# Performance work log

Hardware: AMD Instinct MI355X
Metric: run time of the kernel (lower is better)

## Reference

```python
import jax, jax.numpy as jnp
import numpy as np

NUM_HEADS = 8
NUM_GROUPS = 8
EPS = 1e-5


def group_norm(x, gamma, beta):
    # x: [B, C, H, W], 8 groups over channel dim
    B, C, H, W = x.shape
    xg = x.reshape(B, NUM_GROUPS, C // NUM_GROUPS, H, W)
    mean = xg.mean(axis=(2, 3, 4), keepdims=True)
    var = xg.var(axis=(2, 3, 4), keepdims=True)
    xn = ((xg - mean) * jax.lax.rsqrt(var + EPS)).reshape(B, C, H, W)
    return xn * gamma[None, :, None, None] + beta[None, :, None, None]


def conv1x1(x, w, b):
    # w: [O, C] (1x1 conv kernel squeezed), x: [B, C, H, W]
    return jnp.einsum('oc,bchw->bohw', w, x) + b[None, :, None, None]


def setup_inputs() -> dict:
    key = jax.random.key(0)
    ks = jax.random.split(key, 6)
    B, C, H, W = 16, 512, 32, 32
    x = jax.random.normal(ks[0], (B, C, H, W), dtype=jnp.float32)
    norm_w = jnp.ones((C,), jnp.float32)
    norm_b = jnp.zeros((C,), jnp.float32)
    s = 1.0 / np.sqrt(C)
    qkv_w = jax.random.uniform(ks[1], (3 * C, C), jnp.float32, -s, s)
    qkv_b = jax.random.uniform(ks[2], (3 * C,), jnp.float32, -s, s)
    proj_w = jax.random.uniform(ks[3], (C, C), jnp.float32, -s, s)
    proj_b = jax.random.uniform(ks[4], (C,), jnp.float32, -s, s)
    return {"x": x, "norm_w": norm_w, "norm_b": norm_b,
            "qkv_w": qkv_w, "qkv_b": qkv_b, "proj_w": proj_w, "proj_b": proj_b}


def reference(x, norm_w, norm_b, qkv_w, qkv_b, proj_w, proj_b):
    B, C, H, W = x.shape
    hd = C // NUM_HEADS  # head dim
    h = group_norm(x, norm_w, norm_b)
    qkv = conv1x1(h, qkv_w, qkv_b)                 # [B, 3C, H, W]
    q, k, v = jnp.split(qkv, 3, axis=1)
    q = q.reshape(B, NUM_HEADS, hd, H * W)
    k = k.reshape(B, NUM_HEADS, hd, H * W)
    v = v.reshape(B, NUM_HEADS, hd, H * W)
    scale = hd ** (-0.5)
    attn = jax.nn.softmax(jnp.einsum('bhci,bhcj->bhij', q, k) * scale, axis=-1)
    h = jnp.einsum('bhij,bhcj->bhci', attn, v).reshape(B, C, H, W)
    h = conv1x1(h, proj_w, proj_b)
    return x + h
```

## Files before the change

### kernel.cpp

```cpp
#include <hip/hip_runtime.h>
#include <hip/hip_bf16.h>


typedef __bf16 bf16;
typedef __attribute__((ext_vector_type(8))) __bf16 bf16x8;
typedef __attribute__((ext_vector_type(4))) float f32x4;
typedef __attribute__((ext_vector_type(16))) float f32x16;
typedef __attribute__((ext_vector_type(4))) unsigned int u32x4;

#define SCALE_Q 0.18033688f

__device__ __forceinline__ bf16x8 ld8(const bf16* p) {
    return *reinterpret_cast<const bf16x8*>(p);
}

__device__ __forceinline__ void gl_lds16(const void* g, void* l) {
    __builtin_amdgcn_global_load_lds(
        (const __attribute__((address_space(1))) void*)g,
        (__attribute__((address_space(3))) void*)l, 16, 0, 0);
}

__global__ __launch_bounds__(256) void cvt_weights(const float* __restrict__ qkv_w,
                                                   const float* __restrict__ proj_w,
                                                   bf16* __restrict__ dst) {
    const int N1 = 1536 * 512;
    int i = (blockIdx.x * 256 + threadIdx.x) * 4;
    float4 f = (i < N1) ? *reinterpret_cast<const float4*>(qkv_w + i)
                        : *reinterpret_cast<const float4*>(proj_w + (i - N1));
    dst[i + 0] = (bf16)f.x;
    dst[i + 1] = (bf16)f.y;
    dst[i + 2] = (bf16)f.z;
    dst[i + 3] = (bf16)f.w;
}

__global__ __launch_bounds__(256) void gn_fused(const float* __restrict__ x,
                                                const float* __restrict__ gamma,
                                                const float* __restrict__ beta,
                                                bf16* __restrict__ hnT) {
    int bg = blockIdx.x;
    int b = bg >> 3, g = bg & 7;
    const float* base = x + (size_t)bg * 65536;
    int t = threadIdx.x;
    int wave = t >> 6, lane = t & 63;

    float s = 0.f, sq = 0.f;
    for (int i = t * 4; i < 65536; i += 256 * 4) {
        float4 f = *reinterpret_cast<const float4*>(base + i);
        s += f.x + f.y + f.z + f.w;
        sq += f.x * f.x + f.y * f.y + f.z * f.z + f.w * f.w;
    }
    #pragma unroll
    for (int off = 32; off > 0; off >>= 1) {
        s += __shfl_down(s, off);
        sq += __shfl_down(sq, off);
    }
    __shared__ float ls[4], lq[4];
    __shared__ float2 st;
    if (lane == 0) { ls[wave] = s; lq[wave] = sq; }
    __syncthreads();
    if (t == 0) {
        s = ls[0] + ls[1] + ls[2] + ls[3];
        sq = lq[0] + lq[1] + lq[2] + lq[3];
        float mean = s * (1.f / 65536.f);
        float var = sq * (1.f / 65536.f) - mean * mean;
        st = make_float2(mean, rsqrtf(var + 1e-5f));
    }
    __syncthreads();
    float mean = st.x, rstd = st.y;

    __shared__ float tile[64][65];
    int cl = t & 63;
    float ga = gamma[g * 64 + cl] * rstd;
    float be = beta[g * 64 + cl] - mean * ga;
    for (int pt = 0; pt < 16; pt++) {
        const float* xb = base + pt * 64;
        #pragma unroll
        for (int r = 0; r < 16; r++) {
            int crow = r * 4 + (t >> 6);
            tile[crow][t & 63] = xb[(size_t)crow * 1024 + (t & 63)];
        }
        __syncthreads();
        bf16* ob = hnT + ((size_t)b * 1024 + pt * 64) * 512 + g * 64 + cl;
        #pragma unroll
        for (int r = 0; r < 16; r++) {
            int pl = r * 4 + (t >> 6);
            ob[(size_t)pl * 512] = (bf16)(tile[cl][pl] * ga + be);
        }
        __syncthreads();
    }
}

__device__ __forceinline__ void gemm_stage(const bf16* __restrict__ A,
                                           const bf16* __restrict__ B,
                                           char* smem, int buf,
                                           int m_blk, int n_blk, int k0,
                                           int wave, int lane) {
    char* Al = smem + buf * 32768;
    char* Bl = Al + 16384;
    #pragma unroll
    for (int i = 0; i < 4; i++) {
        int seg = i * 4 + wave;
        int r = seg * 8 + (lane >> 3);
        int cg = (lane & 7) ^ (r & 7);
        gl_lds16((const char*)(A + (size_t)(m_blk + r) * 512 + k0) + cg * 16,
                 Al + seg * 1024);
        gl_lds16((const char*)(B + (size_t)(n_blk + r) * 512 + k0) + cg * 16,
                 Bl + seg * 1024);
    }
}

__device__ __forceinline__ void gemm_compute(const char* smem, int buf,
                                             int wave, int lane,
                                             f32x4 (&acc)[4][4]) {
    const char* Al = smem + buf * 32768;
    const char* Bl = Al + 16384;
    int l15 = lane & 15, hi = lane >> 4;
    int mb = (wave >> 1) * 64, nb = (wave & 1) * 64;
    #pragma unroll
    for (int kc = 0; kc < 2; kc++) {
        int ck = kc * 4 + hi;
        bf16x8 a[4], b[4];
        #pragma unroll
        for (int mf = 0; mf < 4; mf++) {
            int row = mb + mf * 16 + l15;
            a[mf] = *reinterpret_cast<const bf16x8*>(Al + row * 128 + (ck ^ (row & 7)) * 16);
        }
        #pragma unroll
        for (int nf = 0; nf < 4; nf++) {
            int row = nb + nf * 16 + l15;
            b[nf] = *reinterpret_cast<const bf16x8*>(Bl + row * 128 + (ck ^ (row & 7)) * 16);
        }
        #pragma unroll
        for (int mf = 0; mf < 4; mf++)
            #pragma unroll
            for (int nf = 0; nf < 4; nf++)
                acc[mf][nf] = __builtin_amdgcn_mfma_f32_16x16x32_bf16(
                    a[mf], b[nf], acc[mf][nf], 0, 0, 0);
    }
}

#define GEMM_LDS_LOOP(A_, B_, SMEM_)                            \
    f32x4 acc[4][4] = {};                                       \
    {                                                           \
        gemm_stage(A_, B_, SMEM_, 0, m_blk, n_blk, 0, wave, lane); \
        __syncthreads();                                        \
        int buf = 0;                                            \
        for (int ks = 0; ks < 8; ks++) {                        \
            if (ks < 7)                                         \
                gemm_stage(A_, B_, SMEM_, buf ^ 1, m_blk, n_blk, (ks + 1) * 64, wave, lane); \
            gemm_compute(SMEM_, buf, wave, lane, acc);          \
            __syncthreads();                                    \
            buf ^= 1;                                           \
        }                                                       \
    }

__global__ __launch_bounds__(256, 2) void gemm_qkv(const bf16* __restrict__ hnT,
                                                   const bf16* __restrict__ wqkv,
                                                   const float* __restrict__ qkv_b,
                                                   bf16* __restrict__ qk_t,
                                                   bf16* __restrict__ vbuf) {
    __shared__ char smem[65536];
    int b = blockIdx.z;
    int wave = threadIdx.x >> 6, lane = threadIdx.x & 63;
    int l15 = lane & 15;
    int y = blockIdx.y;
    if (y < 8) {
        int m_blk = blockIdx.x * 128;
        int n_blk = y * 128;
        const bf16* A = hnT + (size_t)b * 1024 * 512;
        GEMM_LDS_LOOP(A, wqkv, smem)
        bf16* out = qk_t + (size_t)b * 1024 * 1024;
        int col0 = n_blk + (wave & 1) * 64 + l15;
        int row0 = m_blk + (wave >> 1) * 64 + (lane >> 4) * 4;
        #pragma unroll
        for (int nf = 0; nf < 4; nf++) {
            int col = col0 + nf * 16;
            float bias = qkv_b[col];
            float scl = (col < 512) ? SCALE_Q : 1.0f;
            #pragma unroll
            for (int mf = 0; mf < 4; mf++)
                #pragma unroll
                for (int r = 0; r < 4; r++)
                    out[(size_t)(row0 + mf * 16 + r) * 1024 + col] =
                        (bf16)((acc[mf][nf][r] + bias) * scl);
        }
    } else {
        int m_blk = (y - 8) * 128;
        int n_blk = blockIdx.x * 128;
        const bf16* A = wqkv + (size_t)1024 * 512;
        const bf16* Bm = hnT + (size_t)b * 1024 * 512;
        GEMM_LDS_LOOP(A, Bm, smem)
        bf16* out = vbuf + (size_t)b * 512 * 1024;
        int col0 = n_blk + (wave & 1) * 64 + l15;
        int row0 = m_blk + (wave >> 1) * 64 + (lane >> 4) * 4;
        #pragma unroll
        for (int mf = 0; mf < 4; mf++)
            #pragma unroll
            for (int r = 0; r < 4; r++) {
                int row = row0 + mf * 16 + r;
                float bias = qkv_b[1024 + row];
                #pragma unroll
                for (int nf = 0; nf < 4; nf++)
                    out[(size_t)row * 1024 + col0 + nf * 16] = (bf16)(acc[mf][nf][r] + bias);
            }
    }
}

__global__ __launch_bounds__(256, 2) void gemm_proj(const bf16* __restrict__ wproj,
                                                    const bf16* __restrict__ attnT,
                                                    const float* __restrict__ proj_b,
                                                    const float* __restrict__ x,
                                                    float* __restrict__ out) {
    __shared__ char smem[65536];
    int b = blockIdx.z;
    int wave = threadIdx.x >> 6, lane = threadIdx.x & 63;
    int m_blk = blockIdx.x * 128;
    int n_blk = blockIdx.y * 128;
    const bf16* Bm = attnT + (size_t)b * 1024 * 512;
    GEMM_LDS_LOOP(wproj, Bm, smem)
    const float* xb = x + (size_t)b * 512 * 1024;
    float* ob = out + (size_t)b * 512 * 1024;
    int l15 = lane & 15;
    int col0 = n_blk + (wave & 1) * 64 + l15;
    int row0 = m_blk + (wave >> 1) * 64 + (lane >> 4) * 4;
    #pragma unroll
    for (int mf = 0; mf < 4; mf++)
        #pragma unroll
        for (int r = 0; r < 4; r++) {
            int row = row0 + mf * 16 + r;
            float bias = proj_b[row];
            #pragma unroll
            for (int nf = 0; nf < 4; nf++) {
                size_t idx = (size_t)row * 1024 + col0 + nf * 16;
                ob[idx] = acc[mf][nf][r] + bias + xb[idx];
            }
        }
}

__global__ __launch_bounds__(256, 2) void attn_kernel(const bf16* __restrict__ qk_t,
                                                      const bf16* __restrict__ vbuf,
                                                      bf16* __restrict__ attnT) {
    int flat = blockIdx.x;
    int it = flat >> 7;
    int bh = flat & 127;
    int b = bh >> 3, h = bh & 7;
    int wave = threadIdx.x >> 6, lane = threadIdx.x & 63;
    int l31 = lane & 31, hi = lane >> 5;
    int i0 = it * 128 + wave * 32;
    const bf16* qkb = qk_t + (size_t)b * 1024 * 1024;
    const bf16* kbase = qkb + 512 + h * 64;
    const bf16* vb = vbuf + ((size_t)b * 512 + h * 64) * 1024;

    __shared__ __align__(16) char smem[32768];

    bf16x8 bq[4];
    #pragma unroll
    for (int kc = 0; kc < 4; kc++)
        bq[kc] = ld8(qkb + (size_t)(i0 + l31) * 1024 + h * 64 + kc * 16 + hi * 8);

    f32x16 oacc[2] = {};
    f32x4 l4 = {};

    int srow = wave * 8 + (lane >> 3);
    int cg = (lane & 7) ^ (lane >> 3);
    const char* kp = (const char*)kbase + (size_t)srow * 2048 + cg * 16;
    const char* vp = (const char*)vb + (size_t)srow * 2048 + cg * 16;
    char* ldsK = smem + wave * 1024;

#define ATTN_STAGE(BUFI)                                     \
    {                                                        \
        gl_lds16(kp,         ldsK + (BUFI) * 16384);         \
        gl_lds16(kp + 65536, ldsK + (BUFI) * 16384 + 4096);  \
        gl_lds16(vp,         ldsK + (BUFI) * 16384 + 8192);  \
        gl_lds16(vp + 65536, ldsK + (BUFI) * 16384 + 12288); \
        kp += 131072;                                        \
        vp += 128;                                           \
    }

    int rx = l31 & 7;
    int vaddr[4];
    #pragma unroll
    for (int k = 0; k < 4; k++) vaddr[k] = l31 * 128 + (((k * 2 + hi) ^ rx) * 16);

#define ATTN_COMPUTE(BUFC)                                                              \
    {                                                                                   \
        bf16x8 kf[2][4];                                                                \
        _Pragma("unroll")                                                               \
        for (int jb = 0; jb < 2; jb++)                                                  \
            _Pragma("unroll")                                                           \
            for (int kc = 0; kc < 4; kc++)                                              \
                kf[jb][kc] = *reinterpret_cast<const bf16x8*>(                          \
                    smem + (BUFC) * 16384 + jb * 4096 + vaddr[kc]);                     \
        f32x16 s[2] = {};                                                               \
        _Pragma("unroll")                                                               \
        for (int kc = 0; kc < 4; kc++) {                                                \
            s[0] = __builtin_amdgcn_mfma_f32_32x32x16_bf16(kf[0][kc], bq[kc], s[0], 0, 0, 0); \
            s[1] = __builtin_amdgcn_mfma_f32_32x32x16_bf16(kf[1][kc], bq[kc], s[1], 0, 0, 0); \
        }                                                                               \
        bf16x8 vf[2][4];                                                                \
        _Pragma("unroll")                                                               \
        for (int df = 0; df < 2; df++)                                                  \
            _Pragma("unroll")                                                           \
            for (int ks = 0; ks < 4; ks++)                                              \
                vf[df][ks] = *reinterpret_cast<const bf16x8*>(                          \
                    smem + (BUFC) * 16384 + 8192 + df * 4096 + vaddr[ks]);              \
        unsigned int pk0[2][4], pk1[2][4];                                              \
        _Pragma("unroll")                                                               \
        for (int jb = 0; jb < 2; jb++)                                                  \
            _Pragma("unroll")                                                           \
            for (int m = 0; m < 4; m++) {                                               \
                float e0 = exp2f(s[jb][m * 4 + 0]);                                     \
                float e1 = exp2f(s[jb][m * 4 + 1]);                                     \
                float e2 = exp2f(s[jb][m * 4 + 2]);                                     \
                float e3 = exp2f(s[jb][m * 4 + 3]);                                     \
                f32x4 ev = {e0, e1, e2, e3};                                            \
                l4 += ev;                                                               \
                asm("v_cvt_pk_bf16_f32 %0, %1, %2" : "=v"(pk0[jb][m]) : "v"(e0), "v"(e1)); \
                asm("v_cvt_pk_bf16_f32 %0, %1, %2" : "=v"(pk1[jb][m]) : "v"(e2), "v"(e3)); \
            }                                                                           \
        bf16x8 af[4];                                                                   \
        _Pragma("unroll")                                                               \
        for (int jb = 0; jb < 2; jb++)                                                  \
            _Pragma("unroll")                                                           \
            for (int tt = 0; tt < 2; tt++) {                                            \
                unsigned int a0 = pk0[jb][tt * 2], b0 = pk0[jb][tt * 2 + 1];            \
                unsigned int a1 = pk1[jb][tt * 2], b1 = pk1[jb][tt * 2 + 1];            \
                asm("v_permlane32_swap_b32 %0, %1" : "+v"(a0), "+v"(b0));               \
                asm("v_permlane32_swap_b32 %0, %1" : "+v"(a1), "+v"(b1));               \
                u32x4 w = {a0, a1, b0, b1};                                             \
                af[jb * 2 + tt] = __builtin_bit_cast(bf16x8, w);                        \
            }                                                                           \
        _Pragma("unroll")                                                               \
        for (int ks = 0; ks < 4; ks++) {                                                \
            oacc[0] = __builtin_amdgcn_mfma_f32_32x32x16_bf16(af[ks], vf[0][ks], oacc[0], 0, 0, 0); \
            oacc[1] = __builtin_amdgcn_mfma_f32_32x32x16_bf16(af[ks], vf[1][ks], oacc[1], 0, 0, 0); \
        }                                                                               \
    }

    ATTN_STAGE(0)

    for (int t = 0; t < 16; t += 2) {
        asm volatile("" ::: "memory");
        __builtin_amdgcn_s_barrier();
        ATTN_STAGE(1)
        asm volatile("s_waitcnt vmcnt(4)" ::: "memory");
        __builtin_amdgcn_s_barrier();
        asm volatile("" ::: "memory");
        ATTN_COMPUTE(0)

        asm volatile("" ::: "memory");
        __builtin_amdgcn_s_barrier();
        if (t < 14) {
            ATTN_STAGE(0)
            asm volatile("s_waitcnt vmcnt(4)" ::: "memory");
        } else {
            asm volatile("s_waitcnt vmcnt(0)" ::: "memory");
        }
        __builtin_amdgcn_s_barrier();
        asm volatile("" ::: "memory");
        ATTN_COMPUTE(1)
    }
#undef ATTN_STAGE
#undef ATTN_COMPUTE

    float l_part = (l4[0] + l4[1]) + (l4[2] + l4[3]);
    float lsum = l_part + __shfl_xor(l_part, 32);
    float inv = 1.f / lsum;

    __syncthreads();

    bf16* O_l = (bf16*)smem;
    #pragma unroll
    for (int reg = 0; reg < 16; reg++) {
        int qrow = (reg & 3) + 8 * (reg >> 2) + 4 * hi;
        float iv = __shfl(inv, qrow);
        O_l[(wave * 32 + qrow) * 72 + l31]      = (bf16)(oacc[0][reg] * iv);
        O_l[(wave * 32 + qrow) * 72 + 32 + l31] = (bf16)(oacc[1][reg] * iv);
    }
    __syncthreads();
    {
        int tt = threadIdx.x;
        int il = tt >> 1, half = tt & 1;
        const bf16* lsrc = O_l + il * 72 + half * 32;
        bf16* gdst = attnT + ((size_t)b * 1024 + it * 128 + il) * 512 + h * 64 + half * 32;
        #pragma unroll
        for (int k = 0; k < 4; k++)
            *reinterpret_cast<bf16x8*>(gdst + k * 8) =
                *reinterpret_cast<const bf16x8*>(lsrc + k * 8);
    }
}

extern "C" void kernel_launch(void* const* d_in, const int* in_sizes, int n_in,
                              void* d_out, int out_size, void* d_ws, size_t ws_size,
                              hipStream_t stream) {
    (void)in_sizes; (void)n_in; (void)out_size; (void)ws_size;
    const float* x      = (const float*)d_in[0];
    const float* norm_w = (const float*)d_in[1];
    const float* norm_b = (const float*)d_in[2];
    const float* qkv_w  = (const float*)d_in[3];
    const float* qkv_b  = (const float*)d_in[4];
    const float* proj_w = (const float*)d_in[5];
    const float* proj_b = (const float*)d_in[6];
    float* out = (float*)d_out;

    char* w = (char*)d_ws;
    bf16* wqkv  = (bf16*)w;
    bf16* wproj = wqkv + (size_t)1536 * 512;
    bf16* hnT   = wproj + (size_t)512 * 512;
    bf16* qk_t  = hnT + (size_t)16 * 1024 * 512;
    bf16* vbuf  = qk_t + (size_t)16 * 1024 * 1024;
    bf16* attnT = vbuf + (size_t)16 * 512 * 1024;

    cvt_weights<<<1024, 256, 0, stream>>>(qkv_w, proj_w, wqkv);
    gn_fused<<<128, 256, 0, stream>>>(x, norm_w, norm_b, hnT);
    gemm_qkv<<<dim3(8, 12, 16), 256, 0, stream>>>(hnT, wqkv, qkv_b, qk_t, vbuf);
    attn_kernel<<<1024, 256, 0, stream>>>(qk_t, vbuf, attnT);
    gemm_proj<<<dim3(4, 8, 16), 256, 0, stream>>>(wproj, attnT, proj_b, x, out);
}
```

Measured before the change: 145.9 us.

## Fuse weight conversion into single-pass group norm with LDS-cached bf16 input

Merges the separate weight-conversion kernel into the group-norm kernel, with each of the 128 blocks converting an 8192-element slice of the weights. The group norm now reads x from global memory once instead of twice. Each block stages the whole group as bf16 in 128KB of dynamic LDS with an XOR swizzle, then does the transposed normalized write from LDS. This removes one launch and one read of x, but the large LDS allocation limits occupancy to one block per CU and adds bf16 rounding before normalization.

```diff
diff --git a/kernel.cpp b/kernel.cpp
--- a/kernel.cpp
+++ b/kernel.cpp
@@ -20,73 +20,81 @@
         (__attribute__((address_space(3))) void*)l, 16, 0, 0);
 }
 
-__global__ __launch_bounds__(256) void cvt_weights(const float* __restrict__ qkv_w,
-                                                   const float* __restrict__ proj_w,
-                                                   bf16* __restrict__ dst) {
-    const int N1 = 1536 * 512;
-    int i = (blockIdx.x * 256 + threadIdx.x) * 4;
-    float4 f = (i < N1) ? *reinterpret_cast<const float4*>(qkv_w + i)
-                        : *reinterpret_cast<const float4*>(proj_w + (i - N1));
-    dst[i + 0] = (bf16)f.x;
-    dst[i + 1] = (bf16)f.y;
-    dst[i + 2] = (bf16)f.z;
-    dst[i + 3] = (bf16)f.w;
-}
-
-__global__ __launch_bounds__(256) void gn_fused(const float* __restrict__ x,
-                                                const float* __restrict__ gamma,
-                                                const float* __restrict__ beta,
-                                                bf16* __restrict__ hnT) {
+__global__ __launch_bounds__(256) void gn_cvt_onepass(const float* __restrict__ x,
+                                                      const float* __restrict__ gamma,
+                                                      const float* __restrict__ beta,
+                                                      bf16* __restrict__ hnT,
+                                                      const float* __restrict__ qkv_w,
+                                                      const float* __restrict__ proj_w,
+                                                      bf16* __restrict__ wdst) {
+    extern __shared__ char dsm[];
+    bf16* xc = (bf16*)dsm;
+    float* red = (float*)(dsm + 131072);
     int bg = blockIdx.x;
     int b = bg >> 3, g = bg & 7;
     const float* base = x + (size_t)bg * 65536;
-    int t = threadIdx.x;
-    int wave = t >> 6, lane = t & 63;
+    int t = threadIdx.x, wave = t >> 6, lane = t & 63;
+
+    {
+        const float* src = (bg < 96) ? qkv_w + bg * 8192 : proj_w + (bg - 96) * 8192;
+        bf16* dst = wdst + (size_t)bg * 8192;
+        #pragma unroll
+        for (int k = 0; k < 8; k++) {
+            int i = k * 1024 + t * 4;
+            float4 f = *reinterpret_cast<const float4*>(src + i);
+            dst[i + 0] = (bf16)f.x;
+            dst[i + 1] = (bf16)f.y;
+            dst[i + 2] = (bf16)f.z;
+            dst[i + 3] = (bf16)f.w;
+        }
+    }
 
     float s = 0.f, sq = 0.f;
-    for (int i = t * 4; i < 65536; i += 256 * 4) {
-        float4 f = *reinterpret_cast<const float4*>(base + i);
-        s += f.x + f.y + f.z + f.w;
-        sq += f.x * f.x + f.y * f.y + f.z * f.z + f.w * f.w;
+    {
+        int pc = t >> 1, half = t & 1;
+        for (int k = 0; k < 64; k++) {
+            float4 f = *reinterpret_cast<const float4*>(base + (size_t)k * 1024 + t * 4);
+            s += (f.x + f.y) + (f.z + f.w);
+            sq += (f.x * f.x + f.y * f.y) + (f.z * f.z + f.w * f.w);
+            unsigned pk0, pk1;
+            asm("v_cvt_pk_bf16_f32 %0, %1, %2" : "=v"(pk0) : "v"(f.x), "v"(f.y));
+            asm("v_cvt_pk_bf16_f32 %0, %1, %2" : "=v"(pk1) : "v"(f.z), "v"(f.w));
+            char* dst = (char*)xc + k * 2048 + ((pc ^ (k & 7)) * 16) + half * 8;
+            *reinterpret_cast<uint2*>(dst) = make_uint2(pk0, pk1);
+        }
     }
     #pragma unroll
     for (int off = 32; off > 0; off >>= 1) {
         s += __shfl_down(s, off);
         sq += __shfl_down(sq, off);
     }
-    __shared__ float ls[4], lq[4];
-    __shared__ float2 st;
-    if (lane == 0) { ls[wave] = s; lq[wave] = sq; }
+    if (lane == 0) { red[wave] = s; red[4 + wave] = sq; }
     __syncthreads();
     if (t == 0) {
-        s = ls[0] + ls[1] + ls[2] + ls[3];
-        sq = lq[0] + lq[1] + lq[2] + lq[3];
-        float mean = s * (1.f / 65536.f);
-        float var = sq * (1.f / 65536.f) - mean * mean;
-        st = make_float2(mean, rsqrtf(var + 1e-5f));
+        float S = (red[0] + red[1]) + (red[2] + red[3]);
+        float Q = (red[4] + red[5]) + (red[6] + red[7]);
+        float mean = S * (1.f / 65536.f);
+        float var = Q * (1.f / 65536.f) - mean * mean;
+        red[8] = mean;
+        red[9] = rsqrtf(var + 1e-5f);
     }
     __syncthreads();
-    float mean = st.x, rstd = st.y;
-
-    __shared__ float tile[64][65];
-    int cl = t & 63;
+    float mean = red[8], rstd = red[9];
+
+    int cl = t & 63, quad = t >> 6;
     float ga = gamma[g * 64 + cl] * rstd;
     float be = beta[g * 64 + cl] - mean * ga;
-    for (int pt = 0; pt < 16; pt++) {
-        const float* xb = base + pt * 64;
-        #pragma unroll
-        for (int r = 0; r < 16; r++) {
-            int crow = r * 4 + (t >> 6);
-            tile[crow][t & 63] = xb[(size_t)crow * 1024 + (t & 63)];
-        }
-        __syncthreads();
-        bf16* ob = hnT + ((size_t)b * 1024 + pt * 64) * 512 + g * 64 + cl;
-        #pragma unroll
-        for (int r = 0; r < 16; r++) {
-            int pl = r * 4 + (t >> 6);
-            ob[(size_t)pl * 512] = (bf16)(tile[cl][pl] * ga + be);
-        }
-        __syncthreads();
+    const char* rowbase = (const char*)xc + cl * 2048;
+    int rx = cl & 7;
+    bf16* obase = hnT + (size_t)b * 1024 * 512 + g * 64 + cl;
+    #pragma unroll 4
+    for (int j = 0; j < 32; j++) {
+        int pc = quad + 4 * j;
+        bf16x8 v = *reinterpret_cast<const bf16x8*>(rowbase + ((pc ^ rx) * 16));
+        bf16* ob = obase + (size_t)(pc * 8) * 512;
+        #pragma unroll
+        for (int e = 0; e < 8; e++)
+            ob[(size_t)e * 512] = (bf16)((float)v[e] * ga + be);
     }
 }
 
@@ -411,8 +419,11 @@
     bf16* vbuf  = qk_t + (size_t)16 * 1024 * 1024;
     bf16* attnT = vbuf + (size_t)16 * 512 * 1024;
 
-    cvt_weights<<<1024, 256, 0, stream>>>(qkv_w, proj_w, wqkv);
-    gn_fused<<<128, 256, 0, stream>>>(x, norm_w, norm_b, hnT);
+    const int GN_LDS = 131072 + 64;
+    hipFuncSetAttribute((const void*)gn_cvt_onepass,
+                        hipFuncAttributeMaxDynamicSharedMemorySize, GN_LDS);
+    gn_cvt_onepass<<<128, 256, GN_LDS, stream>>>(x, norm_w, norm_b, hnT,
+                                                 qkv_w, proj_w, wqkv);
     gemm_qkv<<<dim3(8, 12, 16), 256, 0, stream>>>(hnT, wqkv, qkv_b, qk_t, vbuf);
     attn_kernel<<<1024, 256, 0, stream>>>(qk_t, vbuf, attnT);
     gemm_proj<<<dim3(4, 8, 16), 256, 0, stream>>>(wproj, attnT, proj_b, x, out);
```

After: 121.6 us. -16.7%, faster.
